# Optimization experiments

Hardware: AMD Instinct MI355X
Metric: run time of the kernel (lower is better)

Reference implementation:

```python
import jax, jax.numpy as jnp
import numpy as np

N, D_IN, D_OUT, NHEAD = 4096, 512, 128, 4


def setup_inputs() -> dict:
    key = jax.random.key(0)
    k1, k2, k3, k4, k5 = jax.random.split(key, 5)
    adj = jax.random.randint(k1, (N, N), 0, 2).astype(jnp.float32)  # dense binary adjacency
    x = jax.random.normal(k2, (N, D_IN), dtype=jnp.float32)
    W = jax.random.normal(k3, (D_IN, D_OUT), dtype=jnp.float32) * (1.0 / np.sqrt(D_IN))
    attn_l_w = jax.random.normal(k4, (NHEAD, D_OUT), dtype=jnp.float32) * (1.0 / np.sqrt(D_OUT))
    attn_r_w = jax.random.normal(k5, (NHEAD, D_OUT), dtype=jnp.float32) * (1.0 / np.sqrt(D_OUT))
    b = jnp.zeros((D_OUT,), dtype=jnp.float32)
    return {"adj": adj, "x": x, "W": W, "attn_l_w": attn_l_w, "attn_r_w": attn_r_w, "b": b}


def reference(adj, x, W, attn_l_w, attn_r_w, b):
    # h = x @ W : [N, D_OUT]
    h = x @ W
    el = h @ attn_l_w.T  # [N, H]  (nn.Linear(output_dim, nhead, bias=False))
    er = h @ attn_r_w.T  # [N, H]
    # Dense equivalent of nonzero-gather + index_put_ scatter into [N, N, H]:
    # attn[i, j, :] = exp(leaky_relu(el[i] + er[j])) where adj[i, j] != 0, else 0.
    e = el[:, None, :] + er[None, :, :]                      # [N, N, H]
    a = jnp.where(adj[:, :, None] != 0,
                  jnp.exp(jax.nn.leaky_relu(e, negative_slope=0.2)),
                  jnp.zeros((), dtype=e.dtype))              # [N, N, H]
    a = jnp.transpose(a, (0, 2, 1))                          # [N, H, N]
    # F.normalize(p=1, dim=-1): divide by max(L1 row sum, 1e-12); a >= 0 so L1 = sum.
    a = a / jnp.maximum(jnp.sum(a, axis=-1, keepdims=True), 1e-12)
    out = jnp.einsum('nhm,md->nhd', a, h) + b                # [N, H, D_OUT]
    return out.reshape(out.shape[0], -1)                     # flatten heads -> [N, H*D_OUT]
```

## Files before the change

kernel.cpp:

```cpp
#include <hip/hip_runtime.h>

#define NN 4096
#define DIN 512
#define DOUT 128
#define NH 4
#define LOG2E 1.44269504088896340736f

typedef __bf16 bf16x8 __attribute__((ext_vector_type(8)));
typedef float f32x4 __attribute__((ext_vector_type(4)));
typedef unsigned short u16;
typedef u16 u16x8 __attribute__((ext_vector_type(8)));

static __device__ __forceinline__ u16 f2bf(float f) {
  __bf16 h = (__bf16)f;
  return __builtin_bit_cast(u16, h);
}

__global__ __launch_bounds__(512, 1) void precompute_kernel(
    const float* __restrict__ x, const float* __restrict__ W,
    const float* __restrict__ alw, const float* __restrict__ arw,
    u16* __restrict__ hT, float* __restrict__ el, float* __restrict__ erT)
{
  __shared__ __align__(16) float W_lds[128 * 128];
  __shared__ __align__(16) float x_lds[16 * 128];
  const int t = threadIdx.x;
  const int i0 = blockIdx.x * 16;
  const int r = t >> 5;
  const int c = t & 31;
  const int d0 = c * 4;
  float a0 = 0.f, a1 = 0.f, a2 = 0.f, a3 = 0.f;
  for (int kc = 0; kc < 4; ++kc) {
    __syncthreads();
    const float4* Wg4 = (const float4*)(W + kc * (128 * 128));
    float4* Wl4 = (float4*)W_lds;
    #pragma unroll
    for (int q = 0; q < 8; ++q) Wl4[t + q * 512] = Wg4[t + q * 512];
    ((float4*)x_lds)[t] =
        *(const float4*)(x + (size_t)(i0 + r) * DIN + kc * 128 + c * 4);
    __syncthreads();
    #pragma unroll 8
    for (int k = 0; k < 128; ++k) {
      const float xv = x_lds[r * 128 + k];
      const float4 w4 = ((const float4*)W_lds)[k * 32 + c];
      a0 += xv * w4.x; a1 += xv * w4.y; a2 += xv * w4.z; a3 += xv * w4.w;
    }
  }
  const int i = i0 + r;
  hT[(size_t)(d0 + 0) * NN + i] = f2bf(a0);
  hT[(size_t)(d0 + 1) * NN + i] = f2bf(a1);
  hT[(size_t)(d0 + 2) * NN + i] = f2bf(a2);
  hT[(size_t)(d0 + 3) * NN + i] = f2bf(a3);
  float elp[NH], erp[NH];
  #pragma unroll
  for (int hh = 0; hh < NH; ++hh) {
    const float* alr = alw + hh * DOUT + d0;
    const float* arr = arw + hh * DOUT + d0;
    elp[hh] = a0 * alr[0] + a1 * alr[1] + a2 * alr[2] + a3 * alr[3];
    erp[hh] = a0 * arr[0] + a1 * arr[1] + a2 * arr[2] + a3 * arr[3];
  }
  #pragma unroll
  for (int hh = 0; hh < NH; ++hh) {
    #pragma unroll
    for (int off = 1; off < 32; off <<= 1) {
      elp[hh] += __shfl_xor(elp[hh], off);
      erp[hh] += __shfl_xor(erp[hh], off);
    }
  }
  if (c == 0) {
    *(float4*)(el + (size_t)i * NH) =
        make_float4(elp[0] * LOG2E, elp[1] * LOG2E, elp[2] * LOG2E, elp[3] * LOG2E);
    #pragma unroll
    for (int hh = 0; hh < NH; ++hh) erT[(size_t)hh * NN + i] = erp[hh] * LOG2E;
  }
}

__global__ __launch_bounds__(512, 1) void gat_main(
    const float* __restrict__ adj, const u16* __restrict__ hT,
    const float* __restrict__ el, const float* __restrict__ erT,
    const float* __restrict__ bias, float* __restrict__ out)
{
  __shared__ __align__(16) u16 A_lds[64 * 64];
  __shared__ __align__(16) u16 B_lds[128 * 64];
  __shared__ float S_lds[64];
  char* Ab = (char*)A_lds;
  char* Bb = (char*)B_lds;
  const int t = threadIdx.x;
  const int i0 = blockIdx.x * 16;
  const int row = t >> 3;
  const int head = row >> 4;
  const int il = row & 15;
  const int j0 = (t & 7) * 8;
  const float elv = el[(size_t)(i0 + il) * NH + head];
  const float* adjrow = adj + (size_t)(i0 + il) * NN;
  const float* errow = erT + (size_t)head * NN;
  const unsigned a_waddr = (unsigned)(row * 128 + j0 * 2) ^ (unsigned)((row & 7) << 4);
  const int bd = t >> 3;
  const int bk0 = (t & 7) * 8;
  const unsigned b_waddr0 = (unsigned)(bd * 128 + bk0 * 2) ^ (unsigned)((bd & 7) << 4);
  const unsigned b_waddr1 = (unsigned)((bd + 64) * 128 + bk0 * 2) ^ (unsigned)((bd & 7) << 4);
  const int lane = t & 63;
  const int w = t >> 6;
  const int rt = w >> 1;
  const int ch = w & 1;
  const int l15 = lane & 15;
  const int lhi = lane >> 4;
  const int am = rt * 16 + l15;
  const unsigned aswz = (unsigned)((am & 7) << 4);
  f32x4 acc[4];
  #pragma unroll
  for (int ct = 0; ct < 4; ++ct) acc[ct] = (f32x4){0.f, 0.f, 0.f, 0.f};
  float Sp = 0.f;

  for (int jt = 0; jt < 64; ++jt) {
    const int jb = jt * 64;
    __syncthreads();
    const float4 ad0 = *(const float4*)(adjrow + jb + j0);
    const float4 ad1 = *(const float4*)(adjrow + jb + j0 + 4);
    const float4 er0 = *(const float4*)(errow + jb + j0);
    const float4 er1 = *(const float4*)(errow + jb + j0 + 4);
    float av[8];
    {
      float e;
      e = elv + er0.x; av[0] = ad0.x * exp2f(fmaxf(e, 0.f) + 0.2f * fminf(e, 0.f));
      e = elv + er0.y; av[1] = ad0.y * exp2f(fmaxf(e, 0.f) + 0.2f * fminf(e, 0.f));
      e = elv + er0.z; av[2] = ad0.z * exp2f(fmaxf(e, 0.f) + 0.2f * fminf(e, 0.f));
      e = elv + er0.w; av[3] = ad0.w * exp2f(fmaxf(e, 0.f) + 0.2f * fminf(e, 0.f));
      e = elv + er1.x; av[4] = ad1.x * exp2f(fmaxf(e, 0.f) + 0.2f * fminf(e, 0.f));
      e = elv + er1.y; av[5] = ad1.y * exp2f(fmaxf(e, 0.f) + 0.2f * fminf(e, 0.f));
      e = elv + er1.z; av[6] = ad1.z * exp2f(fmaxf(e, 0.f) + 0.2f * fminf(e, 0.f));
      e = elv + er1.w; av[7] = ad1.w * exp2f(fmaxf(e, 0.f) + 0.2f * fminf(e, 0.f));
    }
    Sp += ((av[0] + av[1]) + (av[2] + av[3])) + ((av[4] + av[5]) + (av[6] + av[7]));
    u16x8 pk;
    #pragma unroll
    for (int q = 0; q < 8; ++q) pk[q] = f2bf(av[q]);
    *(u16x8*)(Ab + a_waddr) = pk;
    const u16* hsrc = hT + (size_t)bd * NN + jb + bk0;
    const u16x8 hv0 = *(const u16x8*)hsrc;
    const u16x8 hv1 = *(const u16x8*)(hsrc + (size_t)64 * NN);
    *(u16x8*)(Bb + b_waddr0) = hv0;
    *(u16x8*)(Bb + b_waddr1) = hv1;
    __syncthreads();
    #pragma unroll
    for (int kk = 0; kk < 2; ++kk) {
      const unsigned kbyte = (unsigned)(kk * 64 + lhi * 16);
      const bf16x8 af = *(const bf16x8*)(Ab + (am * 128 + (kbyte ^ aswz)));
      #pragma unroll
      for (int ct = 0; ct < 4; ++ct) {
        const int col = ch * 64 + ct * 16 + l15;
        const bf16x8 bfr = *(const bf16x8*)(Bb + (col * 128 + (kbyte ^ (unsigned)((col & 7) << 4))));
        acc[ct] = __builtin_amdgcn_mfma_f32_16x16x32_bf16(af, bfr, acc[ct], 0, 0, 0);
      }
    }
  }
  Sp += __shfl_xor(Sp, 1);
  Sp += __shfl_xor(Sp, 2);
  Sp += __shfl_xor(Sp, 4);
  if ((t & 7) == 0) S_lds[row] = Sp;
  __syncthreads();
  #pragma unroll
  for (int reg = 0; reg < 4; ++reg) {
    const int mrow = rt * 16 + lhi * 4 + reg;
    const float S = S_lds[mrow];
    const float inv = 1.f / fmaxf(S, 1e-12f);
    const int irow = i0 + (mrow & 15);
    #pragma unroll
    for (int ct = 0; ct < 4; ++ct) {
      const int colp = ch * 64 + ct * 16 + l15;
      out[(size_t)irow * (NH * DOUT) + rt * DOUT + colp] = acc[ct][reg] * inv + bias[colp];
    }
  }
}

extern "C" void kernel_launch(void* const* d_in, const int* in_sizes, int n_in,
                              void* d_out, int out_size, void* d_ws, size_t ws_size,
                              hipStream_t stream) {
  const float* adj = (const float*)d_in[0];
  const float* x   = (const float*)d_in[1];
  const float* W   = (const float*)d_in[2];
  const float* alw = (const float*)d_in[3];
  const float* arw = (const float*)d_in[4];
  const float* bias= (const float*)d_in[5];
  float* out = (float*)d_out;
  char* ws = (char*)d_ws;
  u16*   hT  = (u16*)ws;
  float* el  = (float*)(ws + (1 << 20));
  float* erT = (float*)(ws + (1 << 20) + (64 << 10));
  precompute_kernel<<<256, 512, 0, stream>>>(x, W, alw, arw, hT, el, erT);
  gat_main<<<256, 512, 0, stream>>>(adj, hT, el, erT, bias, out);
}
```

Before: 197.5 us.

## Bit-pack adjacency, MFMA split-bf16 projection, double-buffer and split-K aggregation

Adds a pre-pass that packs the dense float adjacency into one bit per edge, so the main kernel reads 64x fewer adjacency bytes. It replaces the scalar x@W projection with MFMA matmuls that split each operand into high and low bf16 parts to keep near-fp32 accuracy. The main attention kernel gains LDS double-buffering with register prefetch of the next tile. When the workspace is large enough it splits the neighbour dimension in two and adds a reduction kernel for the partial sums and normalisation. In exchange it adds extra launches, a full pass over the float adjacency in the pack step, and a round trip of the partial results through global memory.

```diff
diff --git a/kernel.cpp b/kernel.cpp
--- a/kernel.cpp
+++ b/kernel.cpp
@@ -10,100 +10,167 @@
 typedef float f32x4 __attribute__((ext_vector_type(4)));
 typedef unsigned short u16;
 typedef u16 u16x8 __attribute__((ext_vector_type(8)));
+typedef unsigned long long u64;
 
 static __device__ __forceinline__ u16 f2bf(float f) {
   __bf16 h = (__bf16)f;
   return __builtin_bit_cast(u16, h);
 }
 
-__global__ __launch_bounds__(512, 1) void precompute_kernel(
-    const float* __restrict__ x, const float* __restrict__ W,
-    const float* __restrict__ alw, const float* __restrict__ arw,
-    u16* __restrict__ hT, float* __restrict__ el, float* __restrict__ erT)
-{
-  __shared__ __align__(16) float W_lds[128 * 128];
-  __shared__ __align__(16) float x_lds[16 * 128];
+__global__ __launch_bounds__(256) void pack_adj(const float* __restrict__ adj,
+                                                u64* __restrict__ adjW) {
+  const int t = threadIdx.x;
+  const int lane = t & 63;
+  const int wv = t >> 6;
+  const size_t blk = blockIdx.x;
+  #pragma unroll
+  for (int it = 0; it < 4; ++it) {
+    const size_t wbase = blk * 128 + it * 32 + wv * 8;
+    float v[8];
+    #pragma unroll
+    for (int u = 0; u < 8; ++u) v[u] = adj[(wbase + u) * 64 + lane];
+    #pragma unroll
+    for (int u = 0; u < 8; ++u) {
+      const u64 m = __ballot(v[u] != 0.0f);
+      if (lane == 0) adjW[wbase + u] = m;
+    }
+  }
+}
+
+__global__ __launch_bounds__(256) void prep_wt(const float* __restrict__ W,
+                                               u16* __restrict__ wthi,
+                                               u16* __restrict__ wtlo) {
+  const int n = blockIdx.x;
+  const int t = threadIdx.x;
+  for (int k = t; k < 512; k += 256) {
+    const float w = W[(size_t)k * 128 + n];
+    const __bf16 hi = (__bf16)w;
+    const float lo = w - (float)hi;
+    wthi[(size_t)n * 512 + k] = __builtin_bit_cast(u16, hi);
+    wtlo[(size_t)n * 512 + k] = f2bf(lo);
+  }
+}
+
+__global__ __launch_bounds__(256, 2) void hcompute(
+    const float* __restrict__ x, const u16* __restrict__ wthi,
+    const u16* __restrict__ wtlo, const float* __restrict__ alw,
+    const float* __restrict__ arw, u16* __restrict__ hT,
+    float* __restrict__ el, float* __restrict__ erT) {
+  __shared__ __align__(16) char pool[73728];
+  float* h_lds = (float*)(pool + 8192);
   const int t = threadIdx.x;
   const int i0 = blockIdx.x * 16;
-  const int r = t >> 5;
-  const int c = t & 31;
-  const int d0 = c * 4;
-  float a0 = 0.f, a1 = 0.f, a2 = 0.f, a3 = 0.f;
+  const int lane = t & 63, wv = t >> 6;
+  const int l15 = lane & 15, lhi = lane >> 4;
+  f32x4 acc[2];
+  #pragma unroll
+  for (int nt = 0; nt < 2; ++nt) acc[nt] = (f32x4){0.f, 0.f, 0.f, 0.f};
+  const int xr = t >> 4, xq = (t & 15) * 8;
+  const unsigned x_waddr = (unsigned)(xr * 256 + xq * 2) ^ (unsigned)((xr & 7) << 4);
+  const int wn = t >> 1, wkh = (t & 1) * 64;
+
   for (int kc = 0; kc < 4; ++kc) {
     __syncthreads();
-    const float4* Wg4 = (const float4*)(W + kc * (128 * 128));
-    float4* Wl4 = (float4*)W_lds;
-    #pragma unroll
-    for (int q = 0; q < 8; ++q) Wl4[t + q * 512] = Wg4[t + q * 512];
-    ((float4*)x_lds)[t] =
-        *(const float4*)(x + (size_t)(i0 + r) * DIN + kc * 128 + c * 4);
+    {
+      const float* xsrc = x + (size_t)(i0 + xr) * DIN + kc * 128 + xq;
+      float xv[8];
+      *(float4*)xv = *(const float4*)xsrc;
+      *(float4*)(xv + 4) = *(const float4*)(xsrc + 4);
+      u16x8 xhi, xlo;
+      #pragma unroll
+      for (int q = 0; q < 8; ++q) {
+        const __bf16 hh = (__bf16)xv[q];
+        xhi[q] = __builtin_bit_cast(u16, hh);
+        xlo[q] = f2bf(xv[q] - (float)hh);
+      }
+      *(u16x8*)(pool + x_waddr) = xhi;
+      *(u16x8*)(pool + 4096 + x_waddr) = xlo;
+    }
+    {
+      const u16* whsrc = wthi + (size_t)wn * 512 + kc * 128 + wkh;
+      const u16* wlsrc = wtlo + (size_t)wn * 512 + kc * 128 + wkh;
+      #pragma unroll
+      for (int q = 0; q < 8; ++q) {
+        const unsigned addr =
+            (unsigned)(wn * 256 + (wkh + q * 8) * 2) ^ (unsigned)((wn & 7) << 4);
+        *(u16x8*)(pool + 8192 + addr) = *(const u16x8*)(whsrc + q * 8);
+        *(u16x8*)(pool + 40960 + addr) = *(const u16x8*)(wlsrc + q * 8);
+      }
+    }
     __syncthreads();
-    #pragma unroll 8
-    for (int k = 0; k < 128; ++k) {
-      const float xv = x_lds[r * 128 + k];
-      const float4 w4 = ((const float4*)W_lds)[k * 32 + c];
-      a0 += xv * w4.x; a1 += xv * w4.y; a2 += xv * w4.z; a3 += xv * w4.w;
-    }
-  }
-  const int i = i0 + r;
-  hT[(size_t)(d0 + 0) * NN + i] = f2bf(a0);
-  hT[(size_t)(d0 + 1) * NN + i] = f2bf(a1);
-  hT[(size_t)(d0 + 2) * NN + i] = f2bf(a2);
-  hT[(size_t)(d0 + 3) * NN + i] = f2bf(a3);
-  float elp[NH], erp[NH];
+    #pragma unroll
+    for (int ks = 0; ks < 4; ++ks) {
+      const unsigned kbyte = (unsigned)(ks * 64 + lhi * 16);
+      const unsigned xoff = (unsigned)(l15 * 256) + (kbyte ^ (unsigned)((l15 & 7) << 4));
+      const bf16x8 ah = *(const bf16x8*)(pool + xoff);
+      const bf16x8 al = *(const bf16x8*)(pool + 4096 + xoff);
+      #pragma unroll
+      for (int nt = 0; nt < 2; ++nt) {
+        const int n = wv * 32 + nt * 16 + l15;
+        const unsigned wb = (unsigned)(n * 256) + (kbyte ^ (unsigned)((n & 7) << 4));
+        const bf16x8 bh = *(const bf16x8*)(pool + 8192 + wb);
+        const bf16x8 bl = *(const bf16x8*)(pool + 40960 + wb);
+        acc[nt] = __builtin_amdgcn_mfma_f32_16x16x32_bf16(ah, bh, acc[nt], 0, 0, 0);
+        acc[nt] = __builtin_amdgcn_mfma_f32_16x16x32_bf16(al, bh, acc[nt], 0, 0, 0);
+        acc[nt] = __builtin_amdgcn_mfma_f32_16x16x32_bf16(ah, bl, acc[nt], 0, 0, 0);
+      }
+    }
+  }
+  __syncthreads();
   #pragma unroll
-  for (int hh = 0; hh < NH; ++hh) {
-    const float* alr = alw + hh * DOUT + d0;
-    const float* arr = arw + hh * DOUT + d0;
-    elp[hh] = a0 * alr[0] + a1 * alr[1] + a2 * alr[2] + a3 * alr[3];
-    erp[hh] = a0 * arr[0] + a1 * arr[1] + a2 * arr[2] + a3 * arr[3];
-  }
-  #pragma unroll
-  for (int hh = 0; hh < NH; ++hh) {
-    #pragma unroll
-    for (int off = 1; off < 32; off <<= 1) {
-      elp[hh] += __shfl_xor(elp[hh], off);
-      erp[hh] += __shfl_xor(erp[hh], off);
-    }
-  }
-  if (c == 0) {
-    *(float4*)(el + (size_t)i * NH) =
-        make_float4(elp[0] * LOG2E, elp[1] * LOG2E, elp[2] * LOG2E, elp[3] * LOG2E);
-    #pragma unroll
-    for (int hh = 0; hh < NH; ++hh) erT[(size_t)hh * NN + i] = erp[hh] * LOG2E;
-  }
-}
-
-__global__ __launch_bounds__(512, 1) void gat_main(
-    const float* __restrict__ adj, const u16* __restrict__ hT,
+  for (int nt = 0; nt < 2; ++nt)
+    #pragma unroll
+    for (int reg = 0; reg < 4; ++reg)
+      h_lds[(lhi * 4 + reg) * 132 + wv * 32 + nt * 16 + l15] = acc[nt][reg];
+  __syncthreads();
+  {
+    const int d = t >> 1, ih = (t & 1) * 8;
+    u16x8 hv;
+    #pragma unroll
+    for (int q = 0; q < 8; ++q) hv[q] = f2bf(h_lds[(ih + q) * 132 + d]);
+    *(u16x8*)(hT + (size_t)d * NN + i0 + ih) = hv;
+  }
+  if (t < 128) {
+    const int r = t >> 3, hh = (t >> 1) & 3, side = t & 1;
+    const float* wrow = (side ? arw : alw) + hh * DOUT;
+    float s = 0.f;
+    for (int d = 0; d < 128; ++d) s += h_lds[r * 132 + d] * wrow[d];
+    s *= LOG2E;
+    if (side == 0) el[(size_t)(i0 + r) * NH + hh] = s;
+    else erT[(size_t)hh * NN + i0 + r] = s;
+  }
+}
+
+template <int KSPLIT>
+__global__ __launch_bounds__(512, 4) void gat_main(
+    const unsigned char* __restrict__ adjB, const u16* __restrict__ hT,
     const float* __restrict__ el, const float* __restrict__ erT,
-    const float* __restrict__ bias, float* __restrict__ out)
-{
-  __shared__ __align__(16) u16 A_lds[64 * 64];
-  __shared__ __align__(16) u16 B_lds[128 * 64];
+    const float* __restrict__ bias, float* __restrict__ outp,
+    float* __restrict__ accP, float* __restrict__ SP) {
+  constexpr int NIT = 64 / KSPLIT;
+  __shared__ __align__(16) u16 A_lds[2][64 * 64];
+  __shared__ __align__(16) u16 B_lds[2][128 * 64];
   __shared__ float S_lds[64];
-  char* Ab = (char*)A_lds;
-  char* Bb = (char*)B_lds;
   const int t = threadIdx.x;
-  const int i0 = blockIdx.x * 16;
-  const int row = t >> 3;
-  const int head = row >> 4;
-  const int il = row & 15;
+  const int b = blockIdx.x;
+  const int g = b & 255;
+  const int ks = (KSPLIT > 1) ? (b >> 8) : 0;
+  const int i0 = g * 16;
+  const int row = t >> 3, head = row >> 4, il = row & 15;
   const int j0 = (t & 7) * 8;
   const float elv = el[(size_t)(i0 + il) * NH + head];
-  const float* adjrow = adj + (size_t)(i0 + il) * NN;
-  const float* errow = erT + (size_t)head * NN;
-  const unsigned a_waddr = (unsigned)(row * 128 + j0 * 2) ^ (unsigned)((row & 7) << 4);
-  const int bd = t >> 3;
-  const int bk0 = (t & 7) * 8;
-  const unsigned b_waddr0 = (unsigned)(bd * 128 + bk0 * 2) ^ (unsigned)((bd & 7) << 4);
-  const unsigned b_waddr1 = (unsigned)((bd + 64) * 128 + bk0 * 2) ^ (unsigned)((bd & 7) << 4);
-  const int lane = t & 63;
-  const int w = t >> 6;
-  const int rt = w >> 1;
-  const int ch = w & 1;
-  const int l15 = lane & 15;
-  const int lhi = lane >> 4;
+  const unsigned char* adjrow =
+      adjB + (size_t)(i0 + il) * 512 + (size_t)ks * NIT * 8 + (t & 7);
+  const float* errow = erT + (size_t)head * NN + ks * NIT * 64 + j0;
+  const unsigned a_off = (unsigned)(row * 128 + j0 * 2) ^ (unsigned)((row & 7) << 4);
+  const int bd = t >> 3, bk0 = (t & 7) * 8;
+  const u16* hrow = hT + (size_t)bd * NN + ks * NIT * 64 + bk0;
+  const unsigned b_off0 = (unsigned)(bd * 128 + bk0 * 2) ^ (unsigned)((bd & 7) << 4);
+  const unsigned b_off1 =
+      (unsigned)((bd + 64) * 128 + bk0 * 2) ^ (unsigned)((bd & 7) << 4);
+  const int lane = t & 63, w = t >> 6;
+  const int rt = w >> 1, ch = w & 1;
+  const int l15 = lane & 15, lhi = lane >> 4;
   const int am = rt * 16 + l15;
   const unsigned aswz = (unsigned)((am & 7) << 4);
   f32x4 acc[4];
@@ -111,81 +178,153 @@
   for (int ct = 0; ct < 4; ++ct) acc[ct] = (f32x4){0.f, 0.f, 0.f, 0.f};
   float Sp = 0.f;
 
-  for (int jt = 0; jt < 64; ++jt) {
-    const int jb = jt * 64;
+  auto genTile = [&](unsigned char abv, const float4& ea, const float4& eb,
+                     char* Abuf, char* Bbuf, const u16x8& h0, const u16x8& h1) {
+    float ev[8];
+    *(float4*)ev = ea;
+    *(float4*)(ev + 4) = eb;
+    u16x8 pk;
+    float s = 0.f;
+    #pragma unroll
+    for (int q = 0; q < 8; ++q) {
+      const float e = elv + ev[q];
+      const float ex = exp2f(fmaxf(e, 0.f) + 0.2f * fminf(e, 0.f));
+      const float av = (float)((abv >> q) & 1) * ex;
+      s += av;
+      pk[q] = f2bf(av);
+    }
+    Sp += s;
+    *(u16x8*)(Abuf + a_off) = pk;
+    *(u16x8*)(Bbuf + b_off0) = h0;
+    *(u16x8*)(Bbuf + b_off1) = h1;
+  };
+
+  {
+    const unsigned char ab = adjrow[0];
+    const float4 e0 = *(const float4*)errow;
+    const float4 e1 = *(const float4*)(errow + 4);
+    const u16x8 h0 = *(const u16x8*)hrow;
+    const u16x8 h1 = *(const u16x8*)(hrow + (size_t)64 * NN);
+    genTile(ab, e0, e1, (char*)A_lds[0], (char*)B_lds[0], h0, h1);
+  }
+
+  for (int jt = 0; jt < NIT; ++jt) {
+    const int cur = jt & 1;
     __syncthreads();
-    const float4 ad0 = *(const float4*)(adjrow + jb + j0);
-    const float4 ad1 = *(const float4*)(adjrow + jb + j0 + 4);
-    const float4 er0 = *(const float4*)(errow + jb + j0);
-    const float4 er1 = *(const float4*)(errow + jb + j0 + 4);
-    float av[8];
-    {
-      float e;
-      e = elv + er0.x; av[0] = ad0.x * exp2f(fmaxf(e, 0.f) + 0.2f * fminf(e, 0.f));
-      e = elv + er0.y; av[1] = ad0.y * exp2f(fmaxf(e, 0.f) + 0.2f * fminf(e, 0.f));
-      e = elv + er0.z; av[2] = ad0.z * exp2f(fmaxf(e, 0.f) + 0.2f * fminf(e, 0.f));
-      e = elv + er0.w; av[3] = ad0.w * exp2f(fmaxf(e, 0.f) + 0.2f * fminf(e, 0.f));
-      e = elv + er1.x; av[4] = ad1.x * exp2f(fmaxf(e, 0.f) + 0.2f * fminf(e, 0.f));
-      e = elv + er1.y; av[5] = ad1.y * exp2f(fmaxf(e, 0.f) + 0.2f * fminf(e, 0.f));
-      e = elv + er1.z; av[6] = ad1.z * exp2f(fmaxf(e, 0.f) + 0.2f * fminf(e, 0.f));
-      e = elv + er1.w; av[7] = ad1.w * exp2f(fmaxf(e, 0.f) + 0.2f * fminf(e, 0.f));
-    }
-    Sp += ((av[0] + av[1]) + (av[2] + av[3])) + ((av[4] + av[5]) + (av[6] + av[7]));
-    u16x8 pk;
-    #pragma unroll
-    for (int q = 0; q < 8; ++q) pk[q] = f2bf(av[q]);
-    *(u16x8*)(Ab + a_waddr) = pk;
-    const u16* hsrc = hT + (size_t)bd * NN + jb + bk0;
-    const u16x8 hv0 = *(const u16x8*)hsrc;
-    const u16x8 hv1 = *(const u16x8*)(hsrc + (size_t)64 * NN);
-    *(u16x8*)(Bb + b_waddr0) = hv0;
-    *(u16x8*)(Bb + b_waddr1) = hv1;
-    __syncthreads();
+    unsigned char abn = 0;
+    float4 e0n, e1n;
+    u16x8 h0n, h1n;
+    const bool more = (jt + 1 < NIT);
+    if (more) {
+      abn = adjrow[(jt + 1) * 8];
+      e0n = *(const float4*)(errow + (jt + 1) * 64);
+      e1n = *(const float4*)(errow + (jt + 1) * 64 + 4);
+      h0n = *(const u16x8*)(hrow + (jt + 1) * 64);
+      h1n = *(const u16x8*)(hrow + (jt + 1) * 64 + (size_t)64 * NN);
+    }
+    const char* Abc = (const char*)A_lds[cur];
+    const char* Bbc = (const char*)B_lds[cur];
     #pragma unroll
     for (int kk = 0; kk < 2; ++kk) {
       const unsigned kbyte = (unsigned)(kk * 64 + lhi * 16);
-      const bf16x8 af = *(const bf16x8*)(Ab + (am * 128 + (kbyte ^ aswz)));
+      const bf16x8 af = *(const bf16x8*)(Abc + (am * 128 + (kbyte ^ aswz)));
       #pragma unroll
       for (int ct = 0; ct < 4; ++ct) {
         const int col = ch * 64 + ct * 16 + l15;
-        const bf16x8 bfr = *(const bf16x8*)(Bb + (col * 128 + (kbyte ^ (unsigned)((col & 7) << 4))));
+        const bf16x8 bfr = *(const bf16x8*)(
+            Bbc + (col * 128 + (kbyte ^ (unsigned)((col & 7) << 4))));
         acc[ct] = __builtin_amdgcn_mfma_f32_16x16x32_bf16(af, bfr, acc[ct], 0, 0, 0);
       }
     }
-  }
+    if (more)
+      genTile(abn, e0n, e1n, (char*)A_lds[cur ^ 1], (char*)B_lds[cur ^ 1], h0n, h1n);
+  }
+
   Sp += __shfl_xor(Sp, 1);
   Sp += __shfl_xor(Sp, 2);
   Sp += __shfl_xor(Sp, 4);
-  if ((t & 7) == 0) S_lds[row] = Sp;
-  __syncthreads();
-  #pragma unroll
-  for (int reg = 0; reg < 4; ++reg) {
-    const int mrow = rt * 16 + lhi * 4 + reg;
-    const float S = S_lds[mrow];
-    const float inv = 1.f / fmaxf(S, 1e-12f);
-    const int irow = i0 + (mrow & 15);
-    #pragma unroll
-    for (int ct = 0; ct < 4; ++ct) {
-      const int colp = ch * 64 + ct * 16 + l15;
-      out[(size_t)irow * (NH * DOUT) + rt * DOUT + colp] = acc[ct][reg] * inv + bias[colp];
-    }
-  }
+
+  if (KSPLIT == 1) {
+    if ((t & 7) == 0) S_lds[row] = Sp;
+    __syncthreads();
+    #pragma unroll
+    for (int reg = 0; reg < 4; ++reg) {
+      const int mrow = rt * 16 + lhi * 4 + reg;
+      const float inv = 1.f / fmaxf(S_lds[mrow], 1e-12f);
+      const int irow = i0 + (mrow & 15);
+      #pragma unroll
+      for (int ct = 0; ct < 4; ++ct) {
+        const int colp = ch * 64 + ct * 16 + l15;
+        outp[(size_t)irow * (NH * DOUT) + rt * DOUT + colp] =
+            acc[ct][reg] * inv + bias[colp];
+      }
+    }
+  } else {
+    if ((t & 7) == 0) SP[(size_t)b * 64 + row] = Sp;
+    float* dst = accP + (size_t)b * 8192;
+    #pragma unroll
+    for (int reg = 0; reg < 4; ++reg) {
+      const int mrow = rt * 16 + lhi * 4 + reg;
+      #pragma unroll
+      for (int ct = 0; ct < 4; ++ct) {
+        const int colp = ch * 64 + ct * 16 + l15;
+        dst[mrow * 128 + colp] = acc[ct][reg];
+      }
+    }
+  }
+}
+
+__global__ __launch_bounds__(256) void reduce_norm(
+    const float* __restrict__ accP, const float* __restrict__ SP,
+    const float* __restrict__ bias, float* __restrict__ outp) {
+  const int idx = blockIdx.x * 256 + threadIdx.x;
+  const int o = idx * 4;
+  const int d = o & 127;
+  const int h = (o >> 7) & 3;
+  const int i = o >> 9;
+  const int g = i >> 4;
+  const int m = h * 16 + (i & 15);
+  const float4 p0 = *(const float4*)(accP + (size_t)g * 8192 + m * 128 + d);
+  const float4 p1 = *(const float4*)(accP + (size_t)(256 + g) * 8192 + m * 128 + d);
+  const float S = SP[(size_t)g * 64 + m] + SP[(size_t)(256 + g) * 64 + m];
+  const float inv = 1.f / fmaxf(S, 1e-12f);
+  const float4 bb = *(const float4*)(bias + d);
+  float4 r;
+  r.x = (p0.x + p1.x) * inv + bb.x;
+  r.y = (p0.y + p1.y) * inv + bb.y;
+  r.z = (p0.z + p1.z) * inv + bb.z;
+  r.w = (p0.w + p1.w) * inv + bb.w;
+  *(float4*)(outp + o) = r;
 }
 
 extern "C" void kernel_launch(void* const* d_in, const int* in_sizes, int n_in,
                               void* d_out, int out_size, void* d_ws, size_t ws_size,
                               hipStream_t stream) {
   const float* adj = (const float*)d_in[0];
-  const float* x   = (const float*)d_in[1];
-  const float* W   = (const float*)d_in[2];
+  const float* x = (const float*)d_in[1];
+  const float* W = (const float*)d_in[2];
   const float* alw = (const float*)d_in[3];
   const float* arw = (const float*)d_in[4];
-  const float* bias= (const float*)d_in[5];
+  const float* bias = (const float*)d_in[5];
   float* out = (float*)d_out;
   char* ws = (char*)d_ws;
-  u16*   hT  = (u16*)ws;
-  float* el  = (float*)(ws + (1 << 20));
-  float* erT = (float*)(ws + (1 << 20) + (64 << 10));
-  precompute_kernel<<<256, 512, 0, stream>>>(x, W, alw, arw, hT, el, erT);
-  gat_main<<<256, 512, 0, stream>>>(adj, hT, el, erT, bias, out);
-}
+  u16* hT = (u16*)ws;
+  float* el = (float*)(ws + 0x100000);
+  float* erT = (float*)(ws + 0x110000);
+  unsigned char* adjB = (unsigned char*)(ws + 0x120000);
+  u16* wthi = (u16*)(ws + 0x320000);
+  u16* wtlo = (u16*)(ws + 0x340000);
+  float* accP = (float*)(ws + 0x360000);
+  float* SP = (float*)(ws + 0x1360000);
+  const bool ksplit2 = ws_size >= 0x1380000ull;
+
+  pack_adj<<<2048, 256, 0, stream>>>(adj, (u64*)adjB);
+  prep_wt<<<128, 256, 0, stream>>>(W, wthi, wtlo);
+  hcompute<<<256, 256, 0, stream>>>(x, wthi, wtlo, alw, arw, hT, el, erT);
+  if (ksplit2) {
+    gat_main<2><<<512, 512, 0, stream>>>(adjB, hT, el, erT, bias, out, accP, SP);
+    reduce_norm<<<2048, 256, 0, stream>>>(accP, SP, bias, out);
+  } else {
+    gat_main<1><<<256, 512, 0, stream>>>(adjB, hT, el, erT, bias, out, accP, SP);
+  }
+}
```

Result: faster. 177.3 us (-10.2%).
